# Optimization experiments

Measured on AMD Instinct MI355X. Metric: run time of the kernel, lower is better.

Reference implementation:

```python
import jax, jax.numpy as jnp
import numpy as np

N_NODES = 10000
N_EDGES = 640000
IN_FEATS = 128
OUT_FEATS = 128


def setup_inputs() -> dict:
    key = jax.random.key(0)
    k1, k2, k3, k4, k5 = jax.random.split(key, 5)
    x = jax.random.normal(k1, (N_NODES, IN_FEATS), dtype=jnp.float32)
    src = jax.random.randint(k2, (N_EDGES,), 0, N_NODES, dtype=jnp.int64)
    dst = jax.random.randint(k3, (N_EDGES,), 0, N_NODES, dtype=jnp.int64)
    # nn.Linear(in_feats, out_feats): weight [out, in], bias [out]
    bound = 1.0 / np.sqrt(IN_FEATS)
    W = jax.random.uniform(k4, (OUT_FEATS, IN_FEATS), minval=-bound, maxval=bound, dtype=jnp.float32)
    b = jax.random.uniform(k5, (OUT_FEATS,), minval=-bound, maxval=bound, dtype=jnp.float32)
    return {"x": x, "src": src, "dst": dst, "W": W, "b": b}


def reference(x, src, dst, W, b):
    # DGL GINConv (eps=0, sum aggregator): rst = (1+eps)*x + sum_{j->i} x_j, then Linear
    agg = jax.ops.segment_sum(x[src], dst, num_segments=N_NODES)  # [N, in]
    h = x + agg
    return h @ W.T + b  # [N, out]
```

## Files before the change

### kernel.cpp

```cpp
#include <hip/hip_runtime.h>

#define N_NODES 10000
#define N_EDGES 640000
#define FEATS 128
#define NBKT 625
#define CAPB 2048
#define GSTRIDE 16
#define GEMM_WAVES 1250
#define GEMM_GRID 313
#define P1_BLOCKS 79
#define WCVT_BLOCKS 16
#define CLR_BLOCKS 40

typedef __attribute__((ext_vector_type(8))) short short8;
typedef __attribute__((ext_vector_type(4))) float f32x4;

static __device__ __forceinline__ unsigned short f2bf(float f) {
    unsigned int u = __float_as_uint(f);
    u = (u + 0x7FFFu + ((u >> 16) & 1u)) >> 16;
    return (unsigned short)u;
}
static __device__ __forceinline__ float bf2f(unsigned short h) {
    return __uint_as_float((unsigned int)h << 16);
}

__global__ void prep_kernel(const float* __restrict__ W,
                            unsigned short* __restrict__ wb,
                            int* __restrict__ gcur) {
    int blk = blockIdx.x;
    int tid = threadIdx.x;
    if (blk < WCVT_BLOCKS) {
        int i = blk * 256 + tid;
        float4 v = reinterpret_cast<const float4*>(W)[i];
        ushort4 h;
        h.x = f2bf(v.x); h.y = f2bf(v.y); h.z = f2bf(v.z); h.w = f2bf(v.w);
        reinterpret_cast<ushort4*>(wb)[i] = h;
    } else {
        int i = (blk - WCVT_BLOCKS) * 256 + tid;
        if (i < NBKT * GSTRIDE) gcur[i] = 0;
    }
}

__global__ __launch_bounds__(256) void fused_kernel(const float* __restrict__ x,
                                                    const unsigned short* __restrict__ wb,
                                                    const int* __restrict__ src,
                                                    const int* __restrict__ dst,
                                                    unsigned short* __restrict__ ybf,
                                                    int* __restrict__ gcur,
                                                    int* __restrict__ ebuf) {
    __shared__ int lhist[NBKT];
    __shared__ int sbase[NBKT];
    __shared__ int lcur[NBKT];
    int tid = threadIdx.x;

    if (blockIdx.x < GEMM_GRID) {
        int wave = blockIdx.x * 4 + (tid >> 6);
        if (wave >= GEMM_WAVES) return;
        int lane = tid & 63;
        int mtile = wave >> 1;
        int chalf = (wave & 1) * 64;
        int m0 = mtile * 16;
        int mrow = m0 + (lane & 15);
        int kbase = (lane >> 4) * 8;

        short8 a[4];
        #pragma unroll
        for (int c = 0; c < 4; ++c) {
            const float* xp = x + mrow * FEATS + c * 32 + kbase;
            float4 v0 = *reinterpret_cast<const float4*>(xp);
            float4 v1 = *reinterpret_cast<const float4*>(xp + 4);
            float f[8] = {v0.x, v0.y, v0.z, v0.w, v1.x, v1.y, v1.z, v1.w};
            #pragma unroll
            for (int j = 0; j < 8; ++j) a[c][j] = (short)f2bf(f[j]);
        }

        int nr = lane & 15;
        int rbase = m0 + (lane >> 4) * 4;
        f32x4 accs[4] = {{0.f,0.f,0.f,0.f},{0.f,0.f,0.f,0.f},
                         {0.f,0.f,0.f,0.f},{0.f,0.f,0.f,0.f}};
        #pragma unroll
        for (int c = 0; c < 4; ++c) {
            short8 bfr[4];
            #pragma unroll
            for (int t = 0; t < 4; ++t) {
                int n = chalf + t * 16 + nr;
                bfr[t] = *reinterpret_cast<const short8*>(wb + n * FEATS + c * 32 + kbase);
            }
            #pragma unroll
            for (int t = 0; t < 4; ++t)
                accs[t] = __builtin_amdgcn_mfma_f32_16x16x32_bf16(a[c], bfr[t], accs[t], 0, 0, 0);
        }

        #pragma unroll
        for (int t = 0; t < 4; ++t) {
            int col = chalf + t * 16 + (lane & 15);
            #pragma unroll
            for (int r = 0; r < 4; ++r) {
                ybf[(rbase + r) * FEATS + col] = f2bf(accs[t][r]);
            }
        }
        return;
    }

    int blk = blockIdx.x - GEMM_GRID;
    for (int i = tid; i < NBKT; i += 256) lhist[i] = 0;
    __syncthreads();

    const int4* dst4 = reinterpret_cast<const int4*>(dst);
    const int4* src4 = reinterpret_cast<const int4*>(src);
    int i4base = blk * 2048;

    #pragma unroll
    for (int j = 0; j < 8; ++j) {
        int i4 = i4base + j * 256 + tid;
        if (i4 < N_EDGES / 4) {
            int4 d = dst4[i4];
            atomicAdd(&lhist[d.x >> 4], 1);
            atomicAdd(&lhist[d.y >> 4], 1);
            atomicAdd(&lhist[d.z >> 4], 1);
            atomicAdd(&lhist[d.w >> 4], 1);
        }
    }
    __syncthreads();

    for (int i = tid; i < NBKT; i += 256) {
        int c = lhist[i];
        int base = c ? atomicAdd(&gcur[i * GSTRIDE], c) : 0;
        sbase[i] = i * CAPB + base;
        lcur[i] = 0;
    }
    __syncthreads();

    #pragma unroll
    for (int j = 0; j < 8; ++j) {
        int i4 = i4base + j * 256 + tid;
        if (i4 < N_EDGES / 4) {
            int4 d = dst4[i4];
            int4 s = src4[i4];
            int b0 = d.x >> 4, b1 = d.y >> 4, b2 = d.z >> 4, b3 = d.w >> 4;
            int p0 = atomicAdd(&lcur[b0], 1);
            int p1 = atomicAdd(&lcur[b1], 1);
            int p2 = atomicAdd(&lcur[b2], 1);
            int p3 = atomicAdd(&lcur[b3], 1);
            int a0 = sbase[b0] + p0; if (a0 < (b0 + 1) * CAPB) ebuf[a0] = ((d.x & 15) << 16) | s.x;
            int a1 = sbase[b1] + p1; if (a1 < (b1 + 1) * CAPB) ebuf[a1] = ((d.y & 15) << 16) | s.y;
            int a2 = sbase[b2] + p2; if (a2 < (b2 + 1) * CAPB) ebuf[a2] = ((d.z & 15) << 16) | s.z;
            int a3 = sbase[b3] + p3; if (a3 < (b3 + 1) * CAPB) ebuf[a3] = ((d.w & 15) << 16) | s.w;
        }
    }
}

__global__ __launch_bounds__(1024) void pass2_kernel(const unsigned short* __restrict__ ybf,
                                                     const int* __restrict__ ebuf,
                                                     const int* __restrict__ gcur,
                                                     const float* __restrict__ b,
                                                     float* __restrict__ out) {
    __shared__ int q2[CAPB];
    __shared__ int cnts[16];
    __shared__ int offs[17];
    __shared__ int curs[16];
    int bkt = blockIdx.x;
    int tid = threadIdx.x;

    int cnt = gcur[bkt * GSTRIDE];
    if (cnt > CAPB) cnt = CAPB;
    if (cnt < 0) cnt = 0;
    if (tid < 16) cnts[tid] = 0;
    __syncthreads();

    const int* eb = ebuf + bkt * CAPB;
    for (int i = tid; i < cnt; i += 1024) atomicAdd(&cnts[(eb[i] >> 16) & 15], 1);
    __syncthreads();

    if (tid == 0) {
        int a = 0;
        #pragma unroll
        for (int l = 0; l < 16; ++l) { offs[l] = a; curs[l] = a; a += cnts[l]; }
        offs[16] = a;
    }
    __syncthreads();

    for (int i = tid; i < cnt; i += 1024) {
        int v = eb[i];
        int p = atomicAdd(&curs[(v >> 16) & 15], 1);
        q2[p] = v & 0xFFFF;
    }
    __syncthreads();

    int w = tid >> 6;
    int lane = tid & 63;
    int rg = lane >> 4;
    int fo = lane & 15;
    int s0 = offs[w];
    int s1 = offs[w + 1];

    float acc[8] = {};
    int i = s0;
    for (; i + 8 <= s1; i += 8) {
        int r0 = q2[i + rg];
        int r1 = q2[i + 4 + rg];
        short8 v0 = *reinterpret_cast<const short8*>(ybf + r0 * FEATS + fo * 8);
        short8 v1 = *reinterpret_cast<const short8*>(ybf + r1 * FEATS + fo * 8);
        #pragma unroll
        for (int j = 0; j < 8; ++j) {
            acc[j] += bf2f((unsigned short)v0[j]);
            acc[j] += bf2f((unsigned short)v1[j]);
        }
    }
    for (; i + 4 <= s1; i += 4) {
        int r = q2[i + rg];
        short8 v = *reinterpret_cast<const short8*>(ybf + r * FEATS + fo * 8);
        #pragma unroll
        for (int j = 0; j < 8; ++j) acc[j] += bf2f((unsigned short)v[j]);
    }
    if (i + rg < s1) {
        int r = q2[i + rg];
        short8 v = *reinterpret_cast<const short8*>(ybf + r * FEATS + fo * 8);
        #pragma unroll
        for (int j = 0; j < 8; ++j) acc[j] += bf2f((unsigned short)v[j]);
    }

    #pragma unroll
    for (int j = 0; j < 8; ++j) {
        acc[j] += __shfl_xor(acc[j], 16, 64);
        acc[j] += __shfl_xor(acc[j], 32, 64);
    }

    if (rg == 0) {
        int node = bkt * 16 + w;
        short8 sv = *reinterpret_cast<const short8*>(ybf + node * FEATS + fo * 8);
        float4 b0 = reinterpret_cast<const float4*>(b)[fo * 2];
        float4 b1 = reinterpret_cast<const float4*>(b)[fo * 2 + 1];
        float4 o0, o1;
        o0.x = acc[0] + bf2f((unsigned short)sv[0]) + b0.x;
        o0.y = acc[1] + bf2f((unsigned short)sv[1]) + b0.y;
        o0.z = acc[2] + bf2f((unsigned short)sv[2]) + b0.z;
        o0.w = acc[3] + bf2f((unsigned short)sv[3]) + b0.w;
        o1.x = acc[4] + bf2f((unsigned short)sv[4]) + b1.x;
        o1.y = acc[5] + bf2f((unsigned short)sv[5]) + b1.y;
        o1.z = acc[6] + bf2f((unsigned short)sv[6]) + b1.z;
        o1.w = acc[7] + bf2f((unsigned short)sv[7]) + b1.w;
        float4* op = reinterpret_cast<float4*>(out + node * FEATS + fo * 8);
        op[0] = o0;
        op[1] = o1;
    }
}

extern "C" void kernel_launch(void* const* d_in, const int* in_sizes, int n_in,
                              void* d_out, int out_size, void* d_ws, size_t ws_size,
                              hipStream_t stream) {
    const float* x   = (const float*)d_in[0];
    const int*   src = (const int*)d_in[1];
    const int*   dst = (const int*)d_in[2];
    const float* W   = (const float*)d_in[3];
    const float* b   = (const float*)d_in[4];
    float* out = (float*)d_out;

    unsigned short* wb  = (unsigned short*)d_ws;
    unsigned short* ybf = wb + FEATS * FEATS;
    int* gcur = (int*)(ybf + N_NODES * FEATS);
    int* ebuf = gcur + NBKT * GSTRIDE;

    prep_kernel<<<WCVT_BLOCKS + CLR_BLOCKS, 256, 0, stream>>>(W, wb, gcur);
    fused_kernel<<<GEMM_GRID + P1_BLOCKS, 256, 0, stream>>>(x, wb, src, dst, ybf, gcur, ebuf);
    pass2_kernel<<<NBKT, 1024, 0, stream>>>(ybf, ebuf, gcur, b, out);
}
```

Baseline: 100.2 us.

## Drop prep kernel: per-block local bucket sort, W staged in LDS, gather in pass2

Removes the prep kernel. Each GEMM block now converts W to bf16 into padded shared memory, and the edge partition stops using global atomics into fixed-capacity buckets. Each pass-1 block instead writes its edges into its own sorted chunk, with a prefix-scanned offset table per bucket. Pass2 gathers each bucket's pieces from all 79 chunks into LDS before the local sort. This saves one launch and the global atomic contention, at the cost of redundant W conversion in every GEMM block and extra gather work in pass2; each chunk is also capped at 64 edges per bucket.

```diff
diff --git a/kernel.cpp b/kernel.cpp
--- a/kernel.cpp
+++ b/kernel.cpp
@@ -5,12 +5,12 @@
 #define FEATS 128
 #define NBKT 625
 #define CAPB 2048
-#define GSTRIDE 16
+#define EPB 8192
+#define P1_BLOCKS 79
+#define BSTRIDE (NBKT + 1)
 #define GEMM_WAVES 1250
 #define GEMM_GRID 313
-#define P1_BLOCKS 79
-#define WCVT_BLOCKS 16
-#define CLR_BLOCKS 40
+#define WPAD 136
 
 typedef __attribute__((ext_vector_type(8))) short short8;
 typedef __attribute__((ext_vector_type(4))) float f32x4;
@@ -24,41 +24,34 @@
     return __uint_as_float((unsigned int)h << 16);
 }
 
-__global__ void prep_kernel(const float* __restrict__ W,
-                            unsigned short* __restrict__ wb,
-                            int* __restrict__ gcur) {
-    int blk = blockIdx.x;
-    int tid = threadIdx.x;
-    if (blk < WCVT_BLOCKS) {
-        int i = blk * 256 + tid;
-        float4 v = reinterpret_cast<const float4*>(W)[i];
-        ushort4 h;
-        h.x = f2bf(v.x); h.y = f2bf(v.y); h.z = f2bf(v.z); h.w = f2bf(v.w);
-        reinterpret_cast<ushort4*>(wb)[i] = h;
-    } else {
-        int i = (blk - WCVT_BLOCKS) * 256 + tid;
-        if (i < NBKT * GSTRIDE) gcur[i] = 0;
-    }
-}
-
 __global__ __launch_bounds__(256) void fused_kernel(const float* __restrict__ x,
-                                                    const unsigned short* __restrict__ wb,
+                                                    const float* __restrict__ W,
                                                     const int* __restrict__ src,
                                                     const int* __restrict__ dst,
                                                     unsigned short* __restrict__ ybf,
-                                                    int* __restrict__ gcur,
-                                                    int* __restrict__ ebuf) {
-    __shared__ int lhist[NBKT];
-    __shared__ int sbase[NBKT];
-    __shared__ int lcur[NBKT];
+                                                    int* __restrict__ ebuf,
+                                                    int* __restrict__ boff) {
+    __shared__ union {
+        unsigned short w[128 * WPAD];
+        struct { int lhist[NBKT]; int loff[NBKT + 1]; int lcur[NBKT]; } p;
+    } sm;
     int tid = threadIdx.x;
 
     if (blockIdx.x < GEMM_GRID) {
-        int wave = blockIdx.x * 4 + (tid >> 6);
-        if (wave >= GEMM_WAVES) return;
+        for (int i = tid; i < 4096; i += 256) {
+            float4 v = reinterpret_cast<const float4*>(W)[i];
+            int n = i >> 5, kq = i & 31;
+            ushort4 h;
+            h.x = f2bf(v.x); h.y = f2bf(v.y); h.z = f2bf(v.z); h.w = f2bf(v.w);
+            *reinterpret_cast<ushort4*>(&sm.w[n * WPAD + kq * 4]) = h;
+        }
+        __syncthreads();
+
+        int wv = blockIdx.x * 4 + (tid >> 6);
+        if (wv >= GEMM_WAVES) return;
         int lane = tid & 63;
-        int mtile = wave >> 1;
-        int chalf = (wave & 1) * 64;
+        int mtile = wv >> 1;
+        int chalf = (wv & 1) * 64;
         int m0 = mtile * 16;
         int mrow = m0 + (lane & 15);
         int kbase = (lane >> 4) * 8;
@@ -84,7 +77,7 @@
             #pragma unroll
             for (int t = 0; t < 4; ++t) {
                 int n = chalf + t * 16 + nr;
-                bfr[t] = *reinterpret_cast<const short8*>(wb + n * FEATS + c * 32 + kbase);
+                bfr[t] = *reinterpret_cast<const short8*>(&sm.w[n * WPAD + c * 32 + kbase]);
             }
             #pragma unroll
             for (int t = 0; t < 4; ++t)
@@ -103,75 +96,139 @@
     }
 
     int blk = blockIdx.x - GEMM_GRID;
-    for (int i = tid; i < NBKT; i += 256) lhist[i] = 0;
+    for (int i = tid; i < NBKT; i += 256) sm.p.lhist[i] = 0;
     __syncthreads();
 
     const int4* dst4 = reinterpret_cast<const int4*>(dst);
     const int4* src4 = reinterpret_cast<const int4*>(src);
-    int i4base = blk * 2048;
+    int e0 = blk * EPB;
+    int i40 = e0 / 4;
 
     #pragma unroll
     for (int j = 0; j < 8; ++j) {
-        int i4 = i4base + j * 256 + tid;
+        int i4 = i40 + j * 256 + tid;
         if (i4 < N_EDGES / 4) {
             int4 d = dst4[i4];
-            atomicAdd(&lhist[d.x >> 4], 1);
-            atomicAdd(&lhist[d.y >> 4], 1);
-            atomicAdd(&lhist[d.z >> 4], 1);
-            atomicAdd(&lhist[d.w >> 4], 1);
-        }
-    }
-    __syncthreads();
-
-    for (int i = tid; i < NBKT; i += 256) {
-        int c = lhist[i];
-        int base = c ? atomicAdd(&gcur[i * GSTRIDE], c) : 0;
-        sbase[i] = i * CAPB + base;
-        lcur[i] = 0;
-    }
-    __syncthreads();
+            atomicAdd(&sm.p.lhist[d.x >> 4], 1);
+            atomicAdd(&sm.p.lhist[d.y >> 4], 1);
+            atomicAdd(&sm.p.lhist[d.z >> 4], 1);
+            atomicAdd(&sm.p.lhist[d.w >> 4], 1);
+        }
+    }
+    __syncthreads();
+
+    if (tid < 64) {
+        int base = tid * 10;
+        int loc[10];
+        int s = 0;
+        #pragma unroll
+        for (int j = 0; j < 10; ++j) {
+            int idx = base + j;
+            loc[j] = s;
+            if (idx < NBKT) s += sm.p.lhist[idx];
+        }
+        int v = s;
+        #pragma unroll
+        for (int d = 1; d < 64; d <<= 1) {
+            int u = __shfl_up(v, d, 64);
+            if (tid >= d) v += u;
+        }
+        int pre = v - s;
+        #pragma unroll
+        for (int j = 0; j < 10; ++j) {
+            int idx = base + j;
+            if (idx <= NBKT) {
+                int val = pre + loc[j];
+                sm.p.loff[idx] = val;
+                if (idx < NBKT) sm.p.lcur[idx] = val;
+            }
+        }
+    }
+    __syncthreads();
+
+    for (int i = tid; i < BSTRIDE; i += 256) boff[blk * BSTRIDE + i] = sm.p.loff[i];
 
     #pragma unroll
     for (int j = 0; j < 8; ++j) {
-        int i4 = i4base + j * 256 + tid;
+        int i4 = i40 + j * 256 + tid;
         if (i4 < N_EDGES / 4) {
             int4 d = dst4[i4];
             int4 s = src4[i4];
-            int b0 = d.x >> 4, b1 = d.y >> 4, b2 = d.z >> 4, b3 = d.w >> 4;
-            int p0 = atomicAdd(&lcur[b0], 1);
-            int p1 = atomicAdd(&lcur[b1], 1);
-            int p2 = atomicAdd(&lcur[b2], 1);
-            int p3 = atomicAdd(&lcur[b3], 1);
-            int a0 = sbase[b0] + p0; if (a0 < (b0 + 1) * CAPB) ebuf[a0] = ((d.x & 15) << 16) | s.x;
-            int a1 = sbase[b1] + p1; if (a1 < (b1 + 1) * CAPB) ebuf[a1] = ((d.y & 15) << 16) | s.y;
-            int a2 = sbase[b2] + p2; if (a2 < (b2 + 1) * CAPB) ebuf[a2] = ((d.z & 15) << 16) | s.z;
-            int a3 = sbase[b3] + p3; if (a3 < (b3 + 1) * CAPB) ebuf[a3] = ((d.w & 15) << 16) | s.w;
+            int p0 = atomicAdd(&sm.p.lcur[d.x >> 4], 1);
+            int p1 = atomicAdd(&sm.p.lcur[d.y >> 4], 1);
+            int p2 = atomicAdd(&sm.p.lcur[d.z >> 4], 1);
+            int p3 = atomicAdd(&sm.p.lcur[d.w >> 4], 1);
+            ebuf[e0 + p0] = ((d.x & 15) << 16) | s.x;
+            ebuf[e0 + p1] = ((d.y & 15) << 16) | s.y;
+            ebuf[e0 + p2] = ((d.z & 15) << 16) | s.z;
+            ebuf[e0 + p3] = ((d.w & 15) << 16) | s.w;
         }
     }
 }
 
 __global__ __launch_bounds__(1024) void pass2_kernel(const unsigned short* __restrict__ ybf,
                                                      const int* __restrict__ ebuf,
-                                                     const int* __restrict__ gcur,
+                                                     const int* __restrict__ boff,
                                                      const float* __restrict__ b,
                                                      float* __restrict__ out) {
+    __shared__ int q[CAPB];
     __shared__ int q2[CAPB];
+    __shared__ int chunko[P1_BLOCKS + 1];
+    __shared__ int csrco[P1_BLOCKS];
+    __shared__ int cszs[P1_BLOCKS];
     __shared__ int cnts[16];
     __shared__ int offs[17];
     __shared__ int curs[16];
     int bkt = blockIdx.x;
     int tid = threadIdx.x;
 
-    int cnt = gcur[bkt * GSTRIDE];
+    if (tid < P1_BLOCKS) {
+        int o0 = boff[tid * BSTRIDE + bkt];
+        int o1 = boff[tid * BSTRIDE + bkt + 1];
+        if (o0 < 0) o0 = 0; if (o0 > EPB) o0 = EPB;
+        if (o1 < o0) o1 = o0; if (o1 > EPB) o1 = EPB;
+        int sz = o1 - o0;
+        if (sz > 64) sz = 64;
+        cszs[tid] = sz;
+        csrco[tid] = tid * EPB + o0;
+    }
+    if (tid < 16) cnts[tid] = 0;
+    __syncthreads();
+
+    if (tid < 64) {
+        int i0 = 2 * tid, i1 = 2 * tid + 1;
+        int a0 = (i0 < P1_BLOCKS) ? cszs[i0] : 0;
+        int a1 = (i1 < P1_BLOCKS) ? cszs[i1] : 0;
+        int s = a0 + a1;
+        int v = s;
+        #pragma unroll
+        for (int d = 1; d < 64; d <<= 1) {
+            int u = __shfl_up(v, d, 64);
+            if (tid >= d) v += u;
+        }
+        int pre = v - s;
+        if (i0 <= P1_BLOCKS) chunko[i0] = pre;
+        if (i1 <= P1_BLOCKS) chunko[i1] = pre + a0;
+    }
+    __syncthreads();
+
+    int cnt = chunko[P1_BLOCKS];
     if (cnt > CAPB) cnt = CAPB;
     if (cnt < 0) cnt = 0;
-    if (tid < 16) cnts[tid] = 0;
-    __syncthreads();
-
-    const int* eb = ebuf + bkt * CAPB;
-    for (int i = tid; i < cnt; i += 1024) atomicAdd(&cnts[(eb[i] >> 16) & 15], 1);
-    __syncthreads();
-
+
+    int w = tid >> 6;
+    int lane = tid & 63;
+    for (int c = w; c < P1_BLOCKS; c += 16) {
+        int n = cszs[c], sb = csrco[c], dq = chunko[c];
+        for (int j = lane; j < n; j += 64) {
+            int p = dq + j;
+            if (p < CAPB && p >= 0) q[p] = ebuf[sb + j];
+        }
+    }
+    __syncthreads();
+
+    for (int i = tid; i < cnt; i += 1024) atomicAdd(&cnts[(q[i] >> 16) & 15], 1);
+    __syncthreads();
     if (tid == 0) {
         int a = 0;
         #pragma unroll
@@ -179,16 +236,13 @@
         offs[16] = a;
     }
     __syncthreads();
-
     for (int i = tid; i < cnt; i += 1024) {
-        int v = eb[i];
+        int v = q[i];
         int p = atomicAdd(&curs[(v >> 16) & 15], 1);
         q2[p] = v & 0xFFFF;
     }
     __syncthreads();
 
-    int w = tid >> 6;
-    int lane = tid & 63;
     int rg = lane >> 4;
     int fo = lane & 15;
     int s0 = offs[w];
@@ -256,12 +310,10 @@
     const float* b   = (const float*)d_in[4];
     float* out = (float*)d_out;
 
-    unsigned short* wb  = (unsigned short*)d_ws;
-    unsigned short* ybf = wb + FEATS * FEATS;
-    int* gcur = (int*)(ybf + N_NODES * FEATS);
-    int* ebuf = gcur + NBKT * GSTRIDE;
-
-    prep_kernel<<<WCVT_BLOCKS + CLR_BLOCKS, 256, 0, stream>>>(W, wb, gcur);
-    fused_kernel<<<GEMM_GRID + P1_BLOCKS, 256, 0, stream>>>(x, wb, src, dst, ybf, gcur, ebuf);
-    pass2_kernel<<<NBKT, 1024, 0, stream>>>(ybf, ebuf, gcur, b, out);
-}
+    unsigned short* ybf = (unsigned short*)d_ws;
+    int* ebuf = (int*)(ybf + N_NODES * FEATS);
+    int* boff = ebuf + P1_BLOCKS * EPB;
+
+    fused_kernel<<<GEMM_GRID + P1_BLOCKS, 256, 0, stream>>>(x, W, src, dst, ybf, ebuf, boff);
+    pass2_kernel<<<NBKT, 1024, 0, stream>>>(ybf, ebuf, boff, b, out);
+}
```

New measurement: 98.03 us. -2.1%, faster.
